# Optimization experiments

Hardware: AMD Instinct MI355X
Metric: run time of the kernel (lower is better)

## Reference

```python
import jax, jax.numpy as jnp
import numpy as np

L, B, D, H = 4096, 4, 1024, 16
HD = D // H
SCALAR = 700.0


def setup_inputs() -> dict:
    key = jax.random.key(0)
    ks = jax.random.split(key, 9)
    bound = np.sqrt(6.0 / (D + D)).astype(np.float32)  # xavier_uniform for square weights
    def xavier(k):
        return jax.random.uniform(k, (D, D), jnp.float32, -bound, bound)
    return {
        "input_tensor": jax.random.normal(ks[0], (L, B, D), jnp.float32),
        "num_heads": H,
        "Wq": xavier(ks[1]), "bq": jnp.zeros((D,), jnp.float32),
        "Wk": xavier(ks[2]), "bk": jnp.zeros((D,), jnp.float32),
        "Wv": xavier(ks[3]), "bv": jnp.zeros((D,), jnp.float32),
        "Wo": xavier(ks[4]), "bo": jnp.zeros((D,), jnp.float32),
        "scalar": jnp.asarray(SCALAR, jnp.float32),
    }


def reference(input_tensor, num_heads, Wq, bq, Wk, bk, Wv, bv, Wo, bo, scalar):
    l, b, d = input_tensor.shape
    h = num_heads
    hd = d // h
    scaling = hd ** -0.5
    X = jnp.transpose(input_tensor, (1, 0, 2))  # (b, l, d)
    q = (X @ Wq.T + bq) * scaling
    k = X @ Wk.T + bk
    v = X @ Wv.T + bv
    # split heads: (b, l, h*hd) -> (b, h, l, hd)
    q = q.reshape(b, l, h, hd).transpose(0, 2, 1, 3)
    k = k.reshape(b, l, h, hd).transpose(0, 2, 1, 3)
    v = v.reshape(b, l, h, hd).transpose(0, 2, 1, 3)
    # linear attention: (K^T V) then Q @ (...)  -> O(l * hd^2)
    kv = jnp.einsum('bhld,bhle->bhde', k, v)        # (b, h, hd, hd)
    out = jnp.einsum('bhld,bhde->bhle', q, kv) / scalar  # (b, h, l, hd)
    # faithful to einops '(b h) l d -> b l (d h)': feature layout is (hd, h)
    out = out.transpose(0, 2, 3, 1).reshape(b, l, d)  # (b, l, hd*h)
    out = out @ Wo.T + bo
    return jnp.transpose(out, (1, 0, 2))  # (l, b, d)
```

## Files before the change

kernel.cpp:

```cpp
#include <hip/hip_runtime.h>
#include <stdint.h>
#include <stddef.h>

typedef unsigned short ushort_t;
typedef __attribute__((ext_vector_type(8))) short short8;
typedef __attribute__((ext_vector_type(4))) float f32x4;
typedef __attribute__((ext_vector_type(4))) float float4v;

#define L_DIM 4096
#define B_DIM 4
#define D_DIM 1024
#define H_DIM 16
#define HD_DIM 64
#define M_DIM (L_DIM * B_DIM)

__device__ __forceinline__ float bf2f(ushort_t u) {
    union { unsigned int i; float f; } v; v.i = ((unsigned int)u) << 16; return v.f;
}
__device__ __forceinline__ ushort_t f2bf(float f) {
    union { float f; unsigned int i; } v; v.f = f;
    unsigned int r = v.i + 0x7FFFu + ((v.i >> 16) & 1u);
    return (ushort_t)(r >> 16);
}
__device__ __forceinline__ unsigned int pk2(float a, float b) {
    return (unsigned int)f2bf(a) | ((unsigned int)f2bf(b) << 16);
}
__device__ __forceinline__ void gload16(const ushort_t* g, ushort_t* l) {
    __builtin_amdgcn_global_load_lds(
        (const __attribute__((address_space(1))) unsigned int*)g,
        (__attribute__((address_space(3))) unsigned int*)l, 16, 0, 0);
}

__global__ void detect_kernel(const ushort_t* __restrict__ scal, int* __restrict__ flag)
{
    *flag = (scal[0] == 0) ? 1 : 0;
}

__global__ void convert_b_kernel(const void* bq, const void* bk, const void* bv,
                                 const void* bo, float* __restrict__ bias_f,
                                 const int* __restrict__ flag)
{
    int fl = *flag;
    int idx = blockIdx.x * 256 + threadIdx.x;
    int j = idx >> 10, i = idx & 1023;
    const void* p = (j == 0) ? bq : (j == 1) ? bk : (j == 2) ? bv : bo;
    bias_f[idx] = fl ? ((const float*)p)[i] : bf2f(((const ushort_t*)p)[i]);
}

__global__ void convert_w_kernel(const void* Wk, const void* Wv, const void* Wo,
                                 ushort_t* __restrict__ Wkc, ushort_t* __restrict__ Wvc,
                                 ushort_t* __restrict__ Wpc,
                                 const int* __restrict__ flag)
{
    int fl = *flag;
    int z = blockIdx.z;
    int idx = blockIdx.x * 256 + threadIdx.x;
    const void* src = (z == 0) ? Wk : (z == 1) ? Wv : Wo;
    ushort_t* dst   = (z == 0) ? Wkc : (z == 1) ? Wvc : Wpc;
    size_t sidx;
    if (z < 2) sidx = (size_t)idx;
    else {
        int n = idx >> 10, f = idx & 1023;
        int hh = f >> 6, e = f & 63;
        sidx = (size_t)n * D_DIM + e * H_DIM + hh;
    }
    dst[idx] = fl ? f2bf(((const float*)src)[sidx]) : ((const ushort_t*)src)[sidx];
}

__global__ void convert_x_kernel(const void* __restrict__ X, ushort_t* __restrict__ Xb,
                                 const int* __restrict__ flag)
{
    int fl = *flag;
    size_t i8 = ((size_t)blockIdx.x * 256 + threadIdx.x) * 8;
    if (fl) {
        const float4v* p = (const float4v*)((const float*)X + i8);
        float4v f0 = p[0], f1 = p[1];
        uint4 u;
        u.x = pk2(f0.x, f0.y); u.y = pk2(f0.z, f0.w);
        u.z = pk2(f1.x, f1.y); u.w = pk2(f1.z, f1.w);
        *(uint4*)(Xb + i8) = u;
    } else {
        *(uint4*)(Xb + i8) = *(const uint4*)((const ushort_t*)X + i8);
    }
}

#define BARRIER() asm volatile("s_barrier" ::: "memory")
#define VMWAIT(N) asm volatile("s_waitcnt vmcnt(" #N ")" ::: "memory")

#define STAGE_A(q, kt, dbuf) {                                                 \
    int kc_ = (kt) < 16 ? (kt) : 15;                                           \
    int row_ = ((w & 4) << 5) + (q) * 32 + ((w & 3) << 3) + lrow8;             \
    gload16(A + (size_t)(a_base + (m0 + row_) * astride) * D_DIM               \
                + kc_ * 64 + kcol,                                             \
            sA + (dbuf) * 16384 + row_ * 64 + lcol8); }

#define STAGE_B(o, kt, dbuf) {                                                 \
    int kc_ = (kt) < 16 ? (kt) : 15;                                           \
    int nr_ = (o) * 64 + (w << 3) + lrow8;                                     \
    gload16(W + (size_t)(n0 + nr_) * D_DIM + kc_ * 64 + kcol,                  \
            sB + (dbuf) * 16384 + nr_ * 64 + lcol8); }

#define PROJ_PHASE(S, STAGE0, STAGE1, WAITSTMT)                                \
  {                                                                            \
    short8 af[2][2];                                                           \
    _Pragma("unroll")                                                          \
    for (int j = 0; j < 2; ++j)                                                \
      _Pragma("unroll")                                                        \
      for (int ks = 0; ks < 2; ++ks)                                           \
        af[j][ks] = *(const short8*)&lAc[(awbase + ((S) * 2 + j) * 16) * 64    \
                                         + ((ks * 32 + q8) ^ swz)];            \
    STAGE0; STAGE1;                                                            \
    BARRIER();                                                                 \
    __builtin_amdgcn_s_setprio(1);                                             \
    _Pragma("unroll")                                                          \
    for (int j = 0; j < 2; ++j)                                                \
      _Pragma("unroll")                                                        \
      for (int nt = 0; nt < 4; ++nt)                                           \
        _Pragma("unroll")                                                      \
        for (int ks = 0; ks < 2; ++ks)                                         \
          acc[(S) * 2 + j][nt] = __builtin_amdgcn_mfma_f32_16x16x32_bf16(      \
              af[j][ks], bf[nt][ks], acc[(S) * 2 + j][nt], 0, 0, 0);           \
    __builtin_amdgcn_s_setprio(0);                                             \
    WAITSTMT;                                                                  \
    BARRIER();                                                                 \
  }

__global__ __launch_bounds__(512) void proj_kernel(
    const ushort_t* __restrict__ A, int a_base0, int a_zstride, int astride,
    const ushort_t* __restrict__ W0, int w_z,
    const float* __restrict__ bias0, int b_z,
    void* __restrict__ out, int o_base0, int o_zstride, int ostride,
    const int* __restrict__ flag, int o_dyn)
{
    extern __shared__ ushort_t smem[];
    ushort_t* sA = smem;
    ushort_t* sB = smem + 32768;

    const int z      = blockIdx.z;
    const int a_base = a_base0 + z * a_zstride;
    const int o_base = o_base0 + z * o_zstride;
    const ushort_t* W = W0 + (size_t)z * w_z * (D_DIM * D_DIM);
    const float* bias = bias0 + z * b_z * D_DIM;
    const int ofl  = o_dyn & *flag;
    const int t    = threadIdx.x;
    const int m0   = blockIdx.x * 256;
    const int n0   = blockIdx.y * 256;
    const int w    = t >> 6;
    const int lane = t & 63;
    const int quad = lane >> 4;
    const int l16  = lane & 15;
    const int wm   = w >> 2;
    const int wn   = w & 3;

    const int lrow8 = lane >> 3;
    const int lcol8 = (lane & 7) * 8;
    const int kcol  = (((lane & 7) ^ lrow8) << 3);

    const int awbase = wm * 128 + l16;
    const int bnbase = wn * 64 + l16;
    const int q8     = quad * 8;
    const int swz    = (l16 & 7) << 3;

    f32x4 acc[8][4];
#pragma unroll
    for (int i = 0; i < 8; i++)
#pragma unroll
        for (int j = 0; j < 4; j++) acc[i][j] = f32x4{0.f, 0.f, 0.f, 0.f};

    STAGE_B(0, 0, 0) STAGE_B(1, 0, 0) STAGE_B(2, 0, 0) STAGE_B(3, 0, 0)
    STAGE_A(0, 0, 0) STAGE_A(1, 0, 0) STAGE_A(2, 0, 0) STAGE_A(3, 0, 0)
    STAGE_B(0, 1, 1) STAGE_B(1, 1, 1)
    VMWAIT(4);
    BARRIER();

    for (int c = 0; c < 16; ++c) {
        const int buf = c & 1, nbuf = buf ^ 1;
        const ushort_t* lAc = sA + buf * 16384;
        const ushort_t* lBc = sB + buf * 16384;

        short8 bf[4][2];
#pragma unroll
        for (int nt = 0; nt < 4; ++nt)
#pragma unroll
            for (int ks = 0; ks < 2; ++ks)
                bf[nt][ks] = *(const short8*)&lBc[(bnbase + nt * 16) * 64
                                                  + ((ks * 32 + q8) ^ swz)];

        PROJ_PHASE(0, STAGE_B(2, c + 1, nbuf), STAGE_B(3, c + 1, nbuf), )
        PROJ_PHASE(1, STAGE_A(0, c + 1, nbuf), STAGE_A(1, c + 1, nbuf), VMWAIT(6))
        PROJ_PHASE(2, STAGE_A(2, c + 1, nbuf), STAGE_A(3, c + 1, nbuf), )
        PROJ_PHASE(3, STAGE_B(0, c + 2, buf),  STAGE_B(1, c + 2, buf),  VMWAIT(4))
    }

#pragma unroll
    for (int mt = 0; mt < 8; ++mt) {
#pragma unroll
        for (int nt = 0; nt < 4; ++nt) {
            const int gn = n0 + wn * 64 + nt * 16 + l16;
            const float bv = bias[gn];
#pragma unroll
            for (int i = 0; i < 4; ++i) {
                const int gm = m0 + wm * 128 + mt * 16 + quad * 4 + i;
                const size_t oidx = (size_t)(o_base + gm * ostride) * D_DIM + gn;
                float val = acc[mt][nt][i] + bv;
                if (ofl) {
                    ((float*)out)[oidx] = val;
                } else {
                    float v2 = __shfl_down(val, 1);
                    if (!(l16 & 1))
                        *(unsigned int*)((ushort_t*)out + oidx) = pk2(val, v2);
                }
            }
        }
    }
}

__global__ __launch_bounds__(256) void kv_chunk_kernel(
    const ushort_t* __restrict__ kc, const ushort_t* __restrict__ vc,
    float* __restrict__ part, int lps)
{
    __shared__ ushort_t lkT[64 * 32];
    __shared__ ushort_t lvT[64 * 32];
    const int t    = threadIdx.x;
    const int s    = blockIdx.x;
    const int bh   = blockIdx.y;
    const int b    = bh >> 4, h = bh & 15;
    const int w    = t >> 6;
    const int lane = t & 63, quad = lane >> 4, l16 = lane & 15;

    f32x4 acc[4];
#pragma unroll
    for (int i = 0; i < 4; i++) acc[i] = f32x4{0.f, 0.f, 0.f, 0.f};

    const int niter = lps >> 5;
    for (int kt = 0; kt < niter; kt++) {
        int lcur = s * lps + kt * 32;
        __syncthreads();
#pragma unroll
        for (int i = 0; i < 4; i++) {
            int u  = t + 256 * i;
            int l  = u >> 5;
            int dp = u & 31;
            size_t goff = ((size_t)(lcur + l) * B_DIM + b) * D_DIM + h * HD_DIM + dp * 2;
            unsigned int kw = *(const unsigned int*)(kc + goff);
            unsigned int vw = *(const unsigned int*)(vc + goff);
            lkT[(2 * dp) * 32 + l]     = (ushort_t)kw;
            lkT[(2 * dp + 1) * 32 + l] = (ushort_t)(kw >> 16);
            lvT[(2 * dp) * 32 + l]     = (ushort_t)vw;
            lvT[(2 * dp + 1) * 32 + l] = (ushort_t)(vw >> 16);
        }
        __syncthreads();
        short8 af = *(const short8*)&lvT[(w * 16 + l16) * 32 + quad * 8];
#pragma unroll
        for (int dt = 0; dt < 4; dt++) {
            short8 bfr = *(const short8*)&lkT[(dt * 16 + l16) * 32 + quad * 8];
            acc[dt] = __builtin_amdgcn_mfma_f32_16x16x32_bf16(af, bfr, acc[dt], 0, 0, 0);
        }
    }
#pragma unroll
    for (int dt = 0; dt < 4; dt++) {
#pragma unroll
        for (int i = 0; i < 4; i++) {
            int e = w * 16 + quad * 4 + i;
            int d = dt * 16 + l16;
            part[(((size_t)s * 64 + bh) * 64 + e) * 64 + d] += acc[dt][i];
        }
    }
}

__global__ void kv_reduce_kernel(const float* __restrict__ part,
                                 ushort_t* __restrict__ kvT,
                                 const void* __restrict__ scal,
                                 const int* __restrict__ flag)
{
    int fl = *flag;
    float sc = fl ? *(const float*)scal : bf2f(((const ushort_t*)scal)[0]);
    float inv = 1.0f / sc;
    int idx = blockIdx.x * 256 + threadIdx.x;
    float sum = 0.0f;
#pragma unroll
    for (int s = 0; s < 8; s++) sum += part[((size_t)s << 18) + idx];
    kvT[idx] = f2bf(sum * inv);
}

__global__ __launch_bounds__(256) void wfuse_kernel(
    const void* __restrict__ Wq, const ushort_t* __restrict__ kvT,
    ushort_t* __restrict__ WfT, const int* __restrict__ flag)
{
    __shared__ ushort_t kvL[4096];
    const int fl = *flag;
    const int kt = blockIdx.x, h = blockIdx.y, b = blockIdx.z;
    const int t  = threadIdx.x;
    for (int i = t; i < 2048; i += 256)
        ((unsigned int*)kvL)[i] =
            ((const unsigned int*)(kvT + ((size_t)(b * 16 + h) << 12)))[i];
    __syncthreads();
    const int k  = kt * 128 + (t & 127);
    const int e0 = (t >> 7) * 32;
    float acc[32];
#pragma unroll
    for (int j = 0; j < 32; j++) acc[j] = 0.f;
    for (int d = 0; d < 64; d++) {
        size_t wi = (size_t)(h * 64 + d) * D_DIM + k;
        float wv = 0.125f * (fl ? ((const float*)Wq)[wi]
                                : bf2f(((const ushort_t*)Wq)[wi]));
#pragma unroll
        for (int j = 0; j < 32; j++)
            acc[j] += bf2f(kvL[(e0 + j) * 64 + d]) * wv;
    }
#pragma unroll
    for (int j = 0; j < 32; j++)
        WfT[((size_t)b * 1024 + k) * D_DIM + h * 64 + e0 + j] = f2bf(acc[j]);
}

__global__ void bias_fuse_kernel(const float* __restrict__ bq_f,
                                 const ushort_t* __restrict__ kvT,
                                 float* __restrict__ bfused)
{
    int idx = blockIdx.x * 256 + threadIdx.x;
    int b = idx >> 10, h = (idx >> 6) & 15, e = idx & 63;
    const ushort_t* kvp = kvT + ((size_t)(b * 16 + h) << 12) + e * 64;
    float s = 0.f;
#pragma unroll
    for (int d = 0; d < 64; d++) s += bf2f(kvp[d]) * bq_f[h * 64 + d];
    bfused[idx] = 0.125f * s;
}

__global__ void bias2_kernel(const ushort_t* __restrict__ Wpc,
                             const float* __restrict__ bfused,
                             const float* __restrict__ bo_f,
                             float* __restrict__ b2)
{
    int idx = blockIdx.x * 256 + threadIdx.x;
    int b = idx >> 10, n = idx & 1023;
    const ushort_t* wr = Wpc + (size_t)n * D_DIM;
    const float* bf = bfused + b * 1024;
    float s = 0.f;
    for (int f = 0; f < 1024; f++) s += bf2f(wr[f]) * bf[f];
    b2[idx] = s + bo_f[n];
}

extern "C" void kernel_launch(void* const* d_in, const int* in_sizes, int n_in,
                              void* d_out, int out_size, void* d_ws, size_t ws_size,
                              hipStream_t stream)
{
    const void* X    = d_in[0];
    const void* Wq   = d_in[2];
    const void* bq   = d_in[3];
    const void* Wk   = d_in[4];
    const void* bk   = d_in[5];
    const void* Wv   = d_in[6];
    const void* bv   = d_in[7];
    const void* Wo   = d_in[8];
    const void* bo   = d_in[9];
    const void* scal = d_in[10];

    (void)hipFuncSetAttribute((const void*)proj_kernel,
                              hipFuncAttributeMaxDynamicSharedMemorySize, 131072);

    char* ws = (char*)d_ws;
    int*      flag   = (int*)(ws + 0);
    float*    bias_f = (float*)(ws + 1024);
    float*    bfused = (float*)(ws + 32768);
    float*    b2     = (float*)(ws + 65536);
    float*    bias_z = (float*)(ws + 98304);
    ushort_t* Wkc    = (ushort_t*)(ws + 131072);
    ushort_t* Wvc    = (ushort_t*)(ws + 2228224);
    ushort_t* Wpc    = (ushort_t*)(ws + 4325376);
    ushort_t* kvT    = (ushort_t*)(ws + 6422528);
    float*    part   = (float*)(ws + 6946816);
    ushort_t* Xb     = (ushort_t*)(ws + 15335424);
    ushort_t* kvbuf  = (ushort_t*)(ws + 48889856);
    ushort_t* kc     = kvbuf;
    ushort_t* vc     = kvbuf + (size_t)8192 * D_DIM;
    ushort_t* WfT    = kvbuf;
    ushort_t* W2     = kvbuf + (size_t)4194304;

    detect_kernel<<<1, 1, 0, stream>>>((const ushort_t*)scal, flag);
    convert_b_kernel<<<16, 256, 0, stream>>>(bq, bk, bv, bo, bias_f, flag);
    convert_w_kernel<<<dim3(4096, 1, 3), 256, 0, stream>>>(Wk, Wv, Wo, Wkc, Wvc, Wpc, flag);
    convert_x_kernel<<<8192, 256, 0, stream>>>(X, Xb, flag);
    hipMemsetAsync(part, 0, 8388608, stream);
    hipMemsetAsync(bias_z, 0, 4096, stream);

    for (int c = 0; c < 2; c++) {
        proj_kernel<<<dim3(32, 4, 2), 512, 131072, stream>>>(
            Xb, c * 8192, 0, 1,
            Wkc, 1,
            bias_f + 1024, 1,
            kvbuf, 0, 8192, 1,
            flag, 0);
        kv_chunk_kernel<<<dim3(8, 64), 256, 0, stream>>>(kc, vc, part, 256);
    }
    kv_reduce_kernel<<<1024, 256, 0, stream>>>(part, kvT, scal, flag);

    wfuse_kernel<<<dim3(8, 16, 4), 256, 0, stream>>>(Wq, kvT, WfT, flag);
    bias_fuse_kernel<<<16, 256, 0, stream>>>(bias_f, kvT, bfused);
    bias2_kernel<<<16, 256, 0, stream>>>(Wpc, bfused, bias_f + 3072, b2);

    proj_kernel<<<dim3(4, 4, 4), 512, 131072, stream>>>(
        Wpc, 0, 0, 1,
        WfT, 1,
        bias_z, 0,
        W2, 0, 1024, 1,
        flag, 0);

    proj_kernel<<<dim3(16, 4, 4), 512, 131072, stream>>>(
        Xb, 0, 1, 4,
        W2, 1,
        b2, 1,
        d_out, 0, 1, 4,
        flag, 1);
}
```

Measured before the change: 459.7 us.

## Use MFMA for Wq-kv fusion and smaller-tile GEMM for W2 product

Wq is now converted to bf16 along with the other weights. The scalar FMA wfuse kernel is replaced by an MFMA kernel that stages a transposed Wq tile and the kv matrix in padded LDS. The Wpc×WfT GEMM moves from the large-tile proj_kernel (64 blocks) to a new 128x128-tile kernel with 256 blocks for better CU occupancy. This adds one weight-conversion pass and a new workspace buffer, and the new GEMM kernel has no double buffering.

```diff
diff --git a/kernel.cpp b/kernel.cpp
--- a/kernel.cpp
+++ b/kernel.cpp
@@ -31,6 +31,16 @@
         (__attribute__((address_space(3))) unsigned int*)l, 16, 0, 0);
 }
 
+union U32x4S8 { unsigned int u[4]; short8 s; };
+__device__ __forceinline__ short8 read_frag66(const ushort_t* p) {
+    U32x4S8 r;
+    r.u[0] = *(const unsigned int*)(p + 0);
+    r.u[1] = *(const unsigned int*)(p + 2);
+    r.u[2] = *(const unsigned int*)(p + 4);
+    r.u[3] = *(const unsigned int*)(p + 6);
+    return r.s;
+}
+
 __global__ void detect_kernel(const ushort_t* __restrict__ scal, int* __restrict__ flag)
 {
     *flag = (scal[0] == 0) ? 1 : 0;
@@ -48,17 +58,18 @@
 }
 
 __global__ void convert_w_kernel(const void* Wk, const void* Wv, const void* Wo,
+                                 const void* Wq,
                                  ushort_t* __restrict__ Wkc, ushort_t* __restrict__ Wvc,
-                                 ushort_t* __restrict__ Wpc,
+                                 ushort_t* __restrict__ Wpc, ushort_t* __restrict__ Wqc,
                                  const int* __restrict__ flag)
 {
     int fl = *flag;
     int z = blockIdx.z;
     int idx = blockIdx.x * 256 + threadIdx.x;
-    const void* src = (z == 0) ? Wk : (z == 1) ? Wv : Wo;
-    ushort_t* dst   = (z == 0) ? Wkc : (z == 1) ? Wvc : Wpc;
+    const void* src = (z == 0) ? Wk : (z == 1) ? Wv : (z == 2) ? Wo : Wq;
+    ushort_t* dst   = (z == 0) ? Wkc : (z == 1) ? Wvc : (z == 2) ? Wpc : Wqc;
     size_t sidx;
-    if (z < 2) sidx = (size_t)idx;
+    if (z != 2) sidx = (size_t)idx;
     else {
         int n = idx >> 10, f = idx & 1023;
         int hh = f >> 6, e = f & 63;
@@ -215,6 +226,81 @@
     }
 }
 
+__global__ __launch_bounds__(256) void proj128_kernel(
+    const ushort_t* __restrict__ A, int a_base0, int a_zstride, int astride,
+    const ushort_t* __restrict__ W0, int w_z,
+    const float* __restrict__ bias0, int b_z,
+    void* __restrict__ out, int o_base0, int o_zstride, int ostride,
+    const int* __restrict__ flag, int o_dyn)
+{
+    __shared__ ushort_t lA[128 * 32];
+    __shared__ ushort_t lB[128 * 32];
+    const int z    = blockIdx.z;
+    const int a_base = a_base0 + z * a_zstride;
+    const int o_base = o_base0 + z * o_zstride;
+    const ushort_t* W = W0 + (size_t)z * w_z * (D_DIM * D_DIM);
+    const float* bias = bias0 + z * b_z * D_DIM;
+    const int ofl  = o_dyn & *flag;
+    const int t    = threadIdx.x;
+    const int m0   = blockIdx.x * 128;
+    const int n0   = blockIdx.y * 128;
+    const int w    = t >> 6;
+    const int lane = t & 63;
+    const int quad = lane >> 4;
+    const int l16  = lane & 15;
+    const int wm   = (w >> 1) * 64;
+    const int wn   = (w & 1) * 64;
+
+    const int c0 = t, c1 = t + 256;
+    const int r0 = c0 >> 2, col0 = (c0 & 3) * 8;
+    const int r1 = c1 >> 2, col1 = (c1 & 3) * 8;
+
+    f32x4 acc[4][4];
+#pragma unroll
+    for (int i = 0; i < 4; i++)
+#pragma unroll
+        for (int j = 0; j < 4; j++) acc[i][j] = f32x4{0.f, 0.f, 0.f, 0.f};
+
+    for (int k0 = 0; k0 < D_DIM; k0 += 32) {
+        __syncthreads();
+        gload16(A + (size_t)(a_base + (m0 + r0) * astride) * D_DIM + k0 + col0, &lA[c0 * 8]);
+        gload16(A + (size_t)(a_base + (m0 + r1) * astride) * D_DIM + k0 + col1, &lA[c1 * 8]);
+        gload16(W + (size_t)(n0 + r0) * D_DIM + k0 + col0, &lB[c0 * 8]);
+        gload16(W + (size_t)(n0 + r1) * D_DIM + k0 + col1, &lB[c1 * 8]);
+        __syncthreads();
+        short8 af[4], bfr[4];
+#pragma unroll
+        for (int mt = 0; mt < 4; mt++)
+            af[mt] = *(const short8*)&lA[(wm + mt * 16 + l16) * 32 + quad * 8];
+#pragma unroll
+        for (int nt = 0; nt < 4; nt++)
+            bfr[nt] = *(const short8*)&lB[(wn + nt * 16 + l16) * 32 + quad * 8];
+#pragma unroll
+        for (int mt = 0; mt < 4; mt++)
+#pragma unroll
+            for (int nt = 0; nt < 4; nt++)
+                acc[mt][nt] = __builtin_amdgcn_mfma_f32_16x16x32_bf16(
+                    af[mt], bfr[nt], acc[mt][nt], 0, 0, 0);
+    }
+
+#pragma unroll
+    for (int mt = 0; mt < 4; mt++) {
+#pragma unroll
+        for (int nt = 0; nt < 4; nt++) {
+            int gn = n0 + wn + nt * 16 + l16;
+            float bv = bias[gn];
+#pragma unroll
+            for (int i = 0; i < 4; i++) {
+                int gm = m0 + wm + mt * 16 + quad * 4 + i;
+                size_t oidx = (size_t)(o_base + gm * ostride) * D_DIM + gn;
+                float val = acc[mt][nt][i] + bv;
+                if (ofl) ((float*)out)[oidx] = val;
+                else     ((ushort_t*)out)[oidx] = f2bf(val);
+            }
+        }
+    }
+}
+
 __global__ __launch_bounds__(256) void kv_chunk_kernel(
     const ushort_t* __restrict__ kc, const ushort_t* __restrict__ vc,
     float* __restrict__ part, int lps)
@@ -283,34 +369,83 @@
     kvT[idx] = f2bf(sum * inv);
 }
 
-__global__ __launch_bounds__(256) void wfuse_kernel(
-    const void* __restrict__ Wq, const ushort_t* __restrict__ kvT,
-    ushort_t* __restrict__ WfT, const int* __restrict__ flag)
-{
-    __shared__ ushort_t kvL[4096];
-    const int fl = *flag;
-    const int kt = blockIdx.x, h = blockIdx.y, b = blockIdx.z;
+__global__ __launch_bounds__(256) void wfuse_mfma_kernel(
+    const ushort_t* __restrict__ Wqc, const ushort_t* __restrict__ kvT,
+    ushort_t* __restrict__ WfT)
+{
+    __shared__ ushort_t lA[256][66];
+    __shared__ ushort_t lKV[64][66];
     const int t  = threadIdx.x;
-    for (int i = t; i < 2048; i += 256)
-        ((unsigned int*)kvL)[i] =
-            ((const unsigned int*)(kvT + ((size_t)(b * 16 + h) << 12)))[i];
+    const int k0 = blockIdx.x * 256;
+    const int h  = blockIdx.y, b = blockIdx.z;
+    const int w = t >> 6, lane = t & 63, quad = lane >> 4, l16 = lane & 15;
+    const ushort_t* wq = Wqc + (size_t)h * 64 * D_DIM + k0;
+
+#pragma unroll
+    for (int i = 0; i < 16; ++i) {
+        int u = t + 256 * i;
+        int kp = u & 127, dp = u >> 7;
+        unsigned int w0 = *(const unsigned int*)(wq + (size_t)(2 * dp) * D_DIM + 2 * kp);
+        unsigned int w1 = *(const unsigned int*)(wq + (size_t)(2 * dp + 1) * D_DIM + 2 * kp);
+        *(unsigned int*)&lA[2 * kp][2 * dp]     = (w0 & 0xffffu) | (w1 << 16);
+        *(unsigned int*)&lA[2 * kp + 1][2 * dp] = (w0 >> 16) | (w1 & 0xffff0000u);
+    }
+    const ushort_t* kvp = kvT + ((size_t)(b * 16 + h) << 12);
+#pragma unroll
+    for (int i = 0; i < 2; ++i) {
+        int u = t + 256 * i;
+        int e = u >> 3, d8 = (u & 7) * 8;
+        uint4 v = *(const uint4*)(kvp + e * 64 + d8);
+        *(unsigned int*)&lKV[e][d8]     = v.x;
+        *(unsigned int*)&lKV[e][d8 + 2] = v.y;
+        *(unsigned int*)&lKV[e][d8 + 4] = v.z;
+        *(unsigned int*)&lKV[e][d8 + 6] = v.w;
+    }
     __syncthreads();
-    const int k  = kt * 128 + (t & 127);
-    const int e0 = (t >> 7) * 32;
-    float acc[32];
-#pragma unroll
-    for (int j = 0; j < 32; j++) acc[j] = 0.f;
-    for (int d = 0; d < 64; d++) {
-        size_t wi = (size_t)(h * 64 + d) * D_DIM + k;
-        float wv = 0.125f * (fl ? ((const float*)Wq)[wi]
-                                : bf2f(((const ushort_t*)Wq)[wi]));
-#pragma unroll
-        for (int j = 0; j < 32; j++)
-            acc[j] += bf2f(kvL[(e0 + j) * 64 + d]) * wv;
-    }
-#pragma unroll
-    for (int j = 0; j < 32; j++)
-        WfT[((size_t)b * 1024 + k) * D_DIM + h * 64 + e0 + j] = f2bf(acc[j]);
+
+    short8 bf[4][2];
+#pragma unroll
+    for (int nt = 0; nt < 4; ++nt)
+#pragma unroll
+        for (int ks = 0; ks < 2; ++ks)
+            bf[nt][ks] = read_frag66(&lKV[nt * 16 + l16][ks * 32 + quad * 8]);
+
+    f32x4 acc[4][4];
+#pragma unroll
+    for (int i = 0; i < 4; i++)
+#pragma unroll
+        for (int j = 0; j < 4; j++) acc[i][j] = f32x4{0.f, 0.f, 0.f, 0.f};
+
+#pragma unroll
+    for (int mt = 0; mt < 4; ++mt) {
+        const int krow = w * 64 + mt * 16 + l16;
+        short8 af0 = read_frag66(&lA[krow][quad * 8]);
+        short8 af1 = read_frag66(&lA[krow][32 + quad * 8]);
+#pragma unroll
+        for (int nt = 0; nt < 4; ++nt) {
+            acc[mt][nt] = __builtin_amdgcn_mfma_f32_16x16x32_bf16(
+                af0, bf[nt][0], acc[mt][nt], 0, 0, 0);
+            acc[mt][nt] = __builtin_amdgcn_mfma_f32_16x16x32_bf16(
+                af1, bf[nt][1], acc[mt][nt], 0, 0, 0);
+        }
+    }
+
+#pragma unroll
+    for (int mt = 0; mt < 4; ++mt) {
+#pragma unroll
+        for (int nt = 0; nt < 4; ++nt) {
+            const int gf = h * 64 + nt * 16 + l16;
+#pragma unroll
+            for (int i = 0; i < 4; ++i) {
+                const int gk = k0 + w * 64 + mt * 16 + quad * 4 + i;
+                float val = 0.125f * acc[mt][nt][i];
+                float v2 = __shfl_down(val, 1);
+                if (!(l16 & 1))
+                    *(unsigned int*)(WfT + ((size_t)b * 1024 + gk) * D_DIM + gf)
+                        = pk2(val, v2);
+            }
+        }
+    }
 }
 
 __global__ void bias_fuse_kernel(const float* __restrict__ bq_f,
@@ -375,10 +510,12 @@
     ushort_t* vc     = kvbuf + (size_t)8192 * D_DIM;
     ushort_t* WfT    = kvbuf;
     ushort_t* W2     = kvbuf + (size_t)4194304;
+    ushort_t* Wqc    = (ushort_t*)(ws + 82444288);
 
     detect_kernel<<<1, 1, 0, stream>>>((const ushort_t*)scal, flag);
     convert_b_kernel<<<16, 256, 0, stream>>>(bq, bk, bv, bo, bias_f, flag);
-    convert_w_kernel<<<dim3(4096, 1, 3), 256, 0, stream>>>(Wk, Wv, Wo, Wkc, Wvc, Wpc, flag);
+    convert_w_kernel<<<dim3(4096, 1, 4), 256, 0, stream>>>(Wk, Wv, Wo, Wq,
+                                                           Wkc, Wvc, Wpc, Wqc, flag);
     convert_x_kernel<<<8192, 256, 0, stream>>>(X, Xb, flag);
     hipMemsetAsync(part, 0, 8388608, stream);
     hipMemsetAsync(bias_z, 0, 4096, stream);
@@ -394,11 +531,11 @@
     }
     kv_reduce_kernel<<<1024, 256, 0, stream>>>(part, kvT, scal, flag);
 
-    wfuse_kernel<<<dim3(8, 16, 4), 256, 0, stream>>>(Wq, kvT, WfT, flag);
+    wfuse_mfma_kernel<<<dim3(4, 16, 4), 256, 0, stream>>>(Wqc, kvT, WfT);
     bias_fuse_kernel<<<16, 256, 0, stream>>>(bias_f, kvT, bfused);
     bias2_kernel<<<16, 256, 0, stream>>>(Wpc, bfused, bias_f + 3072, b2);
 
-    proj_kernel<<<dim3(4, 4, 4), 512, 131072, stream>>>(
+    proj128_kernel<<<dim3(8, 8, 4), 256, 0, stream>>>(
         Wpc, 0, 0, 1,
         WfT, 1,
         bias_z, 0,
```

After: 417.0 us. 1.1x faster.
